# Kernel tuning notes

Measured on AMD Instinct MI355X. Metric: run time of the kernel, lower is better.

The kernel has to match this reference:

```python
import jax, jax.numpy as jnp
import numpy as np

KERNEL_SIZE = 3
IGNORE_INDEX = -100


def _unfold(x, k):
    """nn.Unfold(kernel_size=k), stride=1, no padding.
    x: (n, c, h, w) -> (n, c, k*k, L) with L=(h-k+1)*(w-k+1),
    kernel positions in row-major order (matches torch)."""
    n, c, h, w = x.shape
    hp, wp = h - k + 1, w - k + 1
    patches = jnp.stack(
        [x[:, :, i:i + hp, j:j + wp] for i in range(k) for j in range(k)],
        axis=2)  # (n, c, k*k, hp, wp)
    return patches.reshape(n, c, k * k, hp * wp)


def setup_inputs() -> dict:
    key = jax.random.key(0)
    k1, k2 = jax.random.split(key)
    logits = jax.random.normal(k1, (2, 19, 384, 384), dtype=jnp.float32)
    labels = jax.random.randint(k2, (2, 384, 384), 0, 19, dtype=jnp.int32)
    return {"logits": logits, "labels": labels}


def reference(logits, labels):
    n, c, h, w = logits.shape
    # convert_to_one_hot with ignore_index -> zero vector at ignored pixels
    valid = (labels != IGNORE_INDEX)
    oh = jax.nn.one_hot(jnp.where(valid, labels, 0), c, dtype=logits.dtype)
    oh = oh * valid[..., None].astype(logits.dtype)
    oh = jnp.transpose(oh, (0, 3, 1, 2))  # (n, c, h, w)

    lu = _unfold(logits, KERNEL_SIZE)  # (n, c, 9, L)
    yu = _unfold(oh, KERNEL_SIZE)      # (n, c, 9, L)

    aff_map = jnp.einsum('ncal,ncbl->nabl', lu, lu)  # pairwise logit affinity
    lb_map = jnp.einsum('ncal,ncbl->nabl', yu, yu)   # pairwise label affinity

    # BCEWithLogitsLoss(reduction='mean'), numerically stable form
    x, y = aff_map, lb_map
    loss = jnp.mean(jnp.maximum(x, 0) - x * y + jnp.log1p(jnp.exp(-jnp.abs(x))))
    return loss
```

## Files before the change

kernel.cpp:

```cpp
#include <hip/hip_runtime.h>


#define IGNORE_INDEX (-100)

constexpr int Hh = 384, Ww = 384, Cc = 19;
constexpr int HP = 382, WP = 382;
constexpr int TX = 32, TY = 8;
constexpr int LXX = TX + 4;
constexpr int LYY = TY + 2;
constexpr int NBX = Ww / TX, NBY = Hh / TY;
constexpr int NBLK = NBX * NBY * 2;

__device__ __forceinline__ int mult_y(int y, int di) {
    int lo = y - (HP - 1); if (lo < 0) lo = 0;
    int hi = 2 - di;       if (y < hi) hi = y;
    int c = hi - lo + 1;   return c > 0 ? c : 0;
}
__device__ __forceinline__ int mult_x(int x, int dj) {
    int lo = (-dj > 0) ? -dj : 0;
    int lo2 = x - (WP - 1); if (lo2 > lo) lo = lo2;
    int hi = (2 - dj < 2) ? (2 - dj) : 2;
    if (x < hi) hi = x;
    int c = hi - lo + 1;   return c > 0 ? c : 0;
}

__device__ __forceinline__ float bce_term(float x, float y) {
    return fmaxf(x, 0.0f) - x * y + log1pf(expf(-fabsf(x)));
}

__global__ __launch_bounds__(256) void aff_loss_kernel(
        const float* __restrict__ logits, const int* __restrict__ labels,
        double* __restrict__ partial) {
    __shared__ float  sv[LYY * LXX * Cc];
    __shared__ int    sl[LYY * LXX];
    __shared__ double sred[4];

    const int n   = blockIdx.z;
    const int tx0 = blockIdx.x * TX;
    const int ty0 = blockIdx.y * TY;
    const int tid = threadIdx.x;
    const int bid = (blockIdx.z * NBY + blockIdx.y) * NBX + blockIdx.x;

    const float* img = logits + (size_t)n * Cc * Hh * Ww;
    const int*   lab = labels + (size_t)n * Hh * Ww;

    for (int idx = tid; idx < LYY * LXX; idx += 256) {
        int r = idx / LXX, col = idx - r * LXX;
        int gy = ty0 + r;       if (gy > Hh - 1) gy = Hh - 1;
        int gx = tx0 + col - 2; if (gx < 0) gx = 0; if (gx > Ww - 1) gx = Ww - 1;
        sl[idx] = lab[gy * Ww + gx];
        #pragma unroll
        for (int c = 0; c < Cc; ++c)
            sv[idx * Cc + c] = img[(size_t)c * Hh * Ww + gy * Ww + gx];
    }
    __syncthreads();

    const int tx = tid & (TX - 1), ty = tid / TX;
    const int x = tx0 + tx, y = ty0 + ty;
    const int lp_idx = ty * LXX + (tx + 2);

    float v[Cc];
    #pragma unroll
    for (int c = 0; c < Cc; ++c) v[c] = sv[lp_idx * Cc + c];
    const int lp = sl[lp_idx];
    const bool vp = (lp != IGNORE_INDEX);

    double tsum = 0.0;

    {
        float xd = 0.0f;
        #pragma unroll
        for (int c = 0; c < Cc; ++c) xd = fmaf(v[c], v[c], xd);
        float f = (vp ? 0.0f : xd) + log1pf(expf(-xd));
        int w = mult_y(y, 0) * mult_x(x, 0);
        tsum += (double)((float)w * f);
    }

    const int DY[12] = {0, 0, 1, 1, 1, 1, 1, 2, 2, 2, 2, 2};
    const int DX[12] = {1, 2, -2, -1, 0, 1, 2, -2, -1, 0, 1, 2};
    #pragma unroll
    for (int d = 0; d < 12; ++d) {
        const int dy = DY[d], dx = DX[d];
        const int w = mult_y(y, dy) * mult_x(x, dx);
        const int lq_idx = (ty + dy) * LXX + (tx + 2 + dx);
        float xd = 0.0f;
        #pragma unroll
        for (int c = 0; c < Cc; ++c) xd = fmaf(v[c], sv[lq_idx * Cc + c], xd);
        const int lq = sl[lq_idx];
        const float yv = (vp && lq == lp) ? 1.0f : 0.0f;
        float f = bce_term(xd, yv);
        tsum += (double)((float)(2 * w) * f);
    }

    for (int off = 32; off > 0; off >>= 1) tsum += __shfl_down(tsum, off, 64);
    const int wid = tid >> 6;
    if ((tid & 63) == 0) sred[wid] = tsum;
    __syncthreads();
    if (tid == 0)
        partial[bid] = sred[0] + sred[1] + sred[2] + sred[3];
}

__global__ __launch_bounds__(256) void finalize_kernel(
        const double* __restrict__ partial, float* __restrict__ out) {
    __shared__ double sred[4];
    const int tid = threadIdx.x;
    double s = 0.0;
    for (int i = tid; i < NBLK; i += 256) s += partial[i];
    for (int off = 32; off > 0; off >>= 1) s += __shfl_down(s, off, 64);
    if ((tid & 63) == 0) sred[tid >> 6] = s;
    __syncthreads();
    if (tid == 0) {
        double tot = sred[0] + sred[1] + sred[2] + sred[3];
        out[0] = (float)(tot * (1.0 / 23639688.0));
    }
}

extern "C" void kernel_launch(void* const* d_in, const int* in_sizes, int n_in,
                              void* d_out, int out_size, void* d_ws, size_t ws_size,
                              hipStream_t stream) {
    const float* logits = (const float*)d_in[0];
    const int*   labels = (const int*)d_in[1];
    float* out = (float*)d_out;
    double* partial = (double*)d_ws;

    dim3 grid(NBX, NBY, 2);
    aff_loss_kernel<<<grid, 256, 0, stream>>>(logits, labels, partial);
    finalize_kernel<<<1, 256, 0, stream>>>(partial, out);
}
```

Before: 90.40 us.

## Pad channel stride to 20 for float4 LDS access, enlarge tile, use fast softplus

Pads the per-pixel channel vector in shared memory to 20 floats so neighbour vectors can be read with 128-bit LDS loads. It also raises the tile height to 12 rows (384 threads), which reduces halo overhead per block. The BCE term becomes a softplus of a sign-flipped argument built on hardware exp2/log intrinsics, and the x/y multiplicities are precomputed once per thread. The dot products are split across two accumulators for more ILP, at the cost of more registers and approximate transcendentals.

```diff
diff --git a/kernel.cpp b/kernel.cpp
--- a/kernel.cpp
+++ b/kernel.cpp
@@ -4,10 +4,13 @@
 #define IGNORE_INDEX (-100)
 
 constexpr int Hh = 384, Ww = 384, Cc = 19;
+constexpr int HW = Hh * Ww;
 constexpr int HP = 382, WP = 382;
-constexpr int TX = 32, TY = 8;
+constexpr int TX = 32, TY = 12;
+constexpr int NT = TX * TY;
 constexpr int LXX = TX + 4;
 constexpr int LYY = TY + 2;
+constexpr int CS  = 20;
 constexpr int NBX = Ww / TX, NBY = Hh / TY;
 constexpr int NBLK = NBX * NBY * 2;
 
@@ -24,16 +27,18 @@
     int c = hi - lo + 1;   return c > 0 ? c : 0;
 }
 
-__device__ __forceinline__ float bce_term(float x, float y) {
-    return fmaxf(x, 0.0f) - x * y + log1pf(expf(-fabsf(x)));
+__device__ __forceinline__ float softplus(float t) {
+    float e = __builtin_amdgcn_exp2f(-1.4426950408889634f * fabsf(t));
+    float l = __builtin_amdgcn_logf(1.0f + e);
+    return fmaxf(t, 0.0f) + 0.6931471805599453f * l;
 }
 
-__global__ __launch_bounds__(256) void aff_loss_kernel(
+__global__ __launch_bounds__(NT) void aff_loss_kernel(
         const float* __restrict__ logits, const int* __restrict__ labels,
         double* __restrict__ partial) {
-    __shared__ float  sv[LYY * LXX * Cc];
+    __shared__ __align__(16) float sv[LYY * LXX * CS];
     __shared__ int    sl[LYY * LXX];
-    __shared__ double sred[4];
+    __shared__ double sred[NT / 64];
 
     const int n   = blockIdx.z;
     const int tx0 = blockIdx.x * TX;
@@ -41,63 +46,85 @@
     const int tid = threadIdx.x;
     const int bid = (blockIdx.z * NBY + blockIdx.y) * NBX + blockIdx.x;
 
-    const float* img = logits + (size_t)n * Cc * Hh * Ww;
-    const int*   lab = labels + (size_t)n * Hh * Ww;
+    const float* img = logits + (size_t)n * Cc * HW;
+    const int*   lab = labels + (size_t)n * HW;
 
-    for (int idx = tid; idx < LYY * LXX; idx += 256) {
+    for (int idx = tid; idx < LYY * LXX; idx += NT) {
         int r = idx / LXX, col = idx - r * LXX;
         int gy = ty0 + r;       if (gy > Hh - 1) gy = Hh - 1;
         int gx = tx0 + col - 2; if (gx < 0) gx = 0; if (gx > Ww - 1) gx = Ww - 1;
         sl[idx] = lab[gy * Ww + gx];
-        #pragma unroll
-        for (int c = 0; c < Cc; ++c)
-            sv[idx * Cc + c] = img[(size_t)c * Hh * Ww + gy * Ww + gx];
+        const float* s = img + gy * Ww + gx;
+        float4 t0, t1, t2, t3, t4;
+        t0.x = s[0 * HW];  t0.y = s[1 * HW];  t0.z = s[2 * HW];  t0.w = s[3 * HW];
+        t1.x = s[4 * HW];  t1.y = s[5 * HW];  t1.z = s[6 * HW];  t1.w = s[7 * HW];
+        t2.x = s[8 * HW];  t2.y = s[9 * HW];  t2.z = s[10 * HW]; t2.w = s[11 * HW];
+        t3.x = s[12 * HW]; t3.y = s[13 * HW]; t3.z = s[14 * HW]; t3.w = s[15 * HW];
+        t4.x = s[16 * HW]; t4.y = s[17 * HW]; t4.z = s[18 * HW]; t4.w = 0.0f;
+        float4* dst = reinterpret_cast<float4*>(&sv[idx * CS]);
+        dst[0] = t0; dst[1] = t1; dst[2] = t2; dst[3] = t3; dst[4] = t4;
     }
     __syncthreads();
 
-    const int tx = tid & (TX - 1), ty = tid / TX;
+    const int tx = tid & (TX - 1), ty = tid >> 5;
     const int x = tx0 + tx, y = ty0 + ty;
-    const int lp_idx = ty * LXX + (tx + 2);
+    const int ep = ty * LXX + (tx + 2);
 
-    float v[Cc];
+    const float4* P = reinterpret_cast<const float4*>(&sv[ep * CS]);
+    const float4 p0 = P[0], p1 = P[1], p2 = P[2], p3 = P[3], p4 = P[4];
+    const int lp = sl[ep];
+    const bool vp = (lp != IGNORE_INDEX);
+
+    int my_[3], mx_[5];
+    my_[0] = mult_y(y, 0); my_[1] = mult_y(y, 1); my_[2] = mult_y(y, 2);
     #pragma unroll
-    for (int c = 0; c < Cc; ++c) v[c] = sv[lp_idx * Cc + c];
-    const int lp = sl[lp_idx];
-    const bool vp = (lp != IGNORE_INDEX);
+    for (int j = 0; j < 5; ++j) mx_[j] = mult_x(x, j - 2);
 
     double tsum = 0.0;
 
-    {
-        float xd = 0.0f;
-        #pragma unroll
-        for (int c = 0; c < Cc; ++c) xd = fmaf(v[c], v[c], xd);
-        float f = (vp ? 0.0f : xd) + log1pf(expf(-xd));
-        int w = mult_y(y, 0) * mult_x(x, 0);
+    const int DY[13] = {0, 0, 0, 1, 1, 1, 1, 1, 2, 2, 2, 2, 2};
+    const int DX[13] = {0, 1, 2, -2, -1, 0, 1, 2, -2, -1, 0, 1, 2};
+    #pragma unroll
+    for (int d = 0; d < 13; ++d) {
+        const int dy = DY[d], dx = DX[d];
+        float4 b0, b1, b2, b3, b4; int lq;
+        if (d == 0) {
+            b0 = p0; b1 = p1; b2 = p2; b3 = p3; b4 = p4; lq = lp;
+        } else {
+            const int eq = (ty + dy) * LXX + (tx + 2 + dx);
+            const float4* Q = reinterpret_cast<const float4*>(&sv[eq * CS]);
+            b0 = Q[0]; b1 = Q[1]; b2 = Q[2]; b3 = Q[3]; b4 = Q[4];
+            lq = sl[eq];
+        }
+        float xa = p0.x * b0.x, xb = p0.y * b0.y;
+        xa = fmaf(p0.z, b0.z, xa); xb = fmaf(p0.w, b0.w, xb);
+        xa = fmaf(p1.x, b1.x, xa); xb = fmaf(p1.y, b1.y, xb);
+        xa = fmaf(p1.z, b1.z, xa); xb = fmaf(p1.w, b1.w, xb);
+        xa = fmaf(p2.x, b2.x, xa); xb = fmaf(p2.y, b2.y, xb);
+        xa = fmaf(p2.z, b2.z, xa); xb = fmaf(p2.w, b2.w, xb);
+        xa = fmaf(p3.x, b3.x, xa); xb = fmaf(p3.y, b3.y, xb);
+        xa = fmaf(p3.z, b3.z, xa); xb = fmaf(p3.w, b3.w, xb);
+        xa = fmaf(p4.x, b4.x, xa); xb = fmaf(p4.y, b4.y, xb);
+        xa = fmaf(p4.z, b4.z, xa);
+        const float xd = xa + xb;
+
+        const bool same = vp && (lq == lp);
+        const float t = same ? -xd : xd;
+        const float f = softplus(t);
+        const int w = my_[dy] * mx_[dx + 2] * (d == 0 ? 1 : 2);
         tsum += (double)((float)w * f);
-    }
-
-    const int DY[12] = {0, 0, 1, 1, 1, 1, 1, 2, 2, 2, 2, 2};
-    const int DX[12] = {1, 2, -2, -1, 0, 1, 2, -2, -1, 0, 1, 2};
-    #pragma unroll
-    for (int d = 0; d < 12; ++d) {
-        const int dy = DY[d], dx = DX[d];
-        const int w = mult_y(y, dy) * mult_x(x, dx);
-        const int lq_idx = (ty + dy) * LXX + (tx + 2 + dx);
-        float xd = 0.0f;
-        #pragma unroll
-        for (int c = 0; c < Cc; ++c) xd = fmaf(v[c], sv[lq_idx * Cc + c], xd);
-        const int lq = sl[lq_idx];
-        const float yv = (vp && lq == lp) ? 1.0f : 0.0f;
-        float f = bce_term(xd, yv);
-        tsum += (double)((float)(2 * w) * f);
     }
 
     for (int off = 32; off > 0; off >>= 1) tsum += __shfl_down(tsum, off, 64);
     const int wid = tid >> 6;
     if ((tid & 63) == 0) sred[wid] = tsum;
     __syncthreads();
-    if (tid == 0)
-        partial[bid] = sred[0] + sred[1] + sred[2] + sred[3];
+    if (tid == 0) {
+        double s = 0.0;
+        #pragma unroll
+        for (int i = 0; i < NT / 64; ++i) s += sred[i];
+        partial[bid] = s;
+    }
 }
 
 __global__ __launch_bounds__(256) void finalize_kernel(
@@ -124,6 +151,6 @@
     double* partial = (double*)d_ws;
 
     dim3 grid(NBX, NBY, 2);
-    aff_loss_kernel<<<grid, 256, 0, stream>>>(logits, labels, partial);
+    aff_loss_kernel<<<grid, NT, 0, stream>>>(logits, labels, partial);
     finalize_kernel<<<1, 256, 0, stream>>>(partial, out);
 }
```

After: 80.51 us. 1.12x faster.
